# Kernel optimization log

Hardware: AMD Instinct MI355X
Metric: run time of the kernel (lower is better)

## Reference

```python
import jax, jax.numpy as jnp
import numpy as np

V, E, H, D = 10000, 256, 512, 768  # vocab, embed, hidden(=attn), encoder dims
B, T, N = 32, 128, 196


def setup_inputs() -> dict:
    key = jax.random.key(0)
    ks = jax.random.split(key, 16)
    s = 0.02
    inp = {
        "x": jax.random.randint(ks[0], (B, T), 0, V),
        "enc_mem": jax.random.normal(ks[1], (B, N, D), dtype=jnp.float32),
        "enc_mask": jnp.ones((B, N), dtype=jnp.int32),
        # parameters, stored (in, out) so y = x @ W
        "emb_table": jax.random.normal(ks[2], (V, E), dtype=jnp.float32) * s,
        "We": jax.random.normal(ks[3], (D, H), dtype=jnp.float32) * s,   # attn.W_e
        "Wh": jax.random.normal(ks[4], (H, H), dtype=jnp.float32) * s,   # attn.W_h
        "v": jax.random.normal(ks[5], (H,), dtype=jnp.float32) * s,      # attn.v
        "Wih": jax.random.normal(ks[6], (E + D, 4 * H), dtype=jnp.float32) * s,
        "Whh": jax.random.normal(ks[7], (H, 4 * H), dtype=jnp.float32) * s,
        "bih": jnp.zeros((4 * H,), dtype=jnp.float32),
        "bhh": jnp.zeros((4 * H,), dtype=jnp.float32),
        "fcW": jax.random.normal(ks[8], (H, V), dtype=jnp.float32) * s,
        "fcb": jnp.zeros((V,), dtype=jnp.float32),
        "W2h": jax.random.normal(ks[9], (D, H), dtype=jnp.float32) * s,  # enc_to_h
        "b2h": jnp.zeros((H,), dtype=jnp.float32),
        "W2c": jax.random.normal(ks[10], (D, H), dtype=jnp.float32) * s,  # enc_to_c
        "b2c": jnp.zeros((H,), dtype=jnp.float32),
    }
    return inp


def _decode(x, enc_mem, enc_mask, emb_table, We, Wh, v, Wih, Whh, bih, bhh,
            fcW, fcb, W2h, b2h, W2c, b2c):
    emb = emb_table[x]                       # (B,T,E); dropout=0 (eval)
    pooled = enc_mem.mean(axis=1)            # (B,D)
    h = jnp.tanh(pooled @ W2h + b2h)         # init_hidden
    c = jnp.tanh(pooled @ W2c + b2c)
    Ke = jnp.einsum('bnd,dh->bnh', enc_mem, We)  # precompute W_e(enc_mem)
    neg = jnp.float32(-1e9)
    mask0 = (enc_mask == 0)

    def step(carry, e_t):
        h, c = carry
        energy = jnp.tanh((h @ Wh)[:, None, :] + Ke)        # (B,N,H)
        scores = jnp.einsum('bnh,h->bn', energy, v)         # (B,N)
        scores = jnp.where(mask0, neg, scores)
        alpha = jax.nn.softmax(scores, axis=-1)
        context = jnp.einsum('bn,bnd->bd', alpha, enc_mem)  # (B,D)
        lstm_in = jnp.concatenate([e_t, context], axis=-1)  # (B,E+D)
        gates = lstm_in @ Wih + bih + h @ Whh + bhh         # (B,4H)
        i_g, f_g, g_g, o_g = jnp.split(gates, 4, axis=-1)   # torch order i,f,g,o
        c_new = jax.nn.sigmoid(f_g) * c + jax.nn.sigmoid(i_g) * jnp.tanh(g_g)
        h_new = jax.nn.sigmoid(o_g) * jnp.tanh(c_new)
        logit = h_new @ fcW + fcb                           # (B,V)
        return (h_new, c_new), logit

    (h, c), logits_t = jax.lax.scan(step, (h, c), jnp.swapaxes(emb, 0, 1))
    logits = jnp.swapaxes(logits_t, 0, 1)                   # (B,T,V)
    return logits, h, c


def reference(x, enc_mem, enc_mask, emb_table, We, Wh, v, Wih, Whh, bih, bhh,
              fcW, fcb, W2h, b2h, W2c, b2c):
    return _decode(x, enc_mem, enc_mask, emb_table, We, Wh, v, Wih, Whh,
                   bih, bhh, fcW, fcb, W2h, b2h, W2c, b2c)
```

## Files before the change

kernel.cpp:

```cpp
#include <hip/hip_runtime.h>

typedef unsigned short u16;
typedef __attribute__((ext_vector_type(8))) short short8;
typedef __attribute__((ext_vector_type(4))) float f32x4;
typedef __attribute__((ext_vector_type(4))) unsigned int u32x4;

#define B_  32
#define T_  128
#define N_  196
#define D_  768
#define E_  256
#define H_  512
#define V_  10000
#define G4H 2048
#define NBLK 256
#define BH  (B_ * H_)

#define O_ENCBF 0UL
#define O_WHP   9633792UL
#define O_WHHT  10158080UL
#define O_WIHDT 12255232UL
#define O_KE    15400960UL
#define O_GEMB  21823488UL
#define O_BSUM  38600704UL
#define O_CT    38608896UL
#define O_HIST  38674432UL
#define O_HX    42868736UL
#define O_HX2   42999808UL
#define O_HWX   43065344UL
#define O_CTXA  43130880UL
#define O_DEN   43229184UL
#define O_BARS  43229696UL
#define O_REL   43231744UL

__device__ __forceinline__ float b2f(u16 u) {
  union { unsigned i; float f; } c; c.i = ((unsigned)u) << 16; return c.f;
}
__device__ __forceinline__ u16 f2b(float f) {
  unsigned u = __float_as_uint(f);
  unsigned r = (u + 0x7fffu + ((u >> 16) & 1u)) >> 16;
  return (u16)r;
}
__device__ __forceinline__ float fast_tanh(float x) {
  float e = __expf(2.f * x);
  return 1.f - 2.f * __builtin_amdgcn_rcpf(e + 1.f);
}
__device__ __forceinline__ float sigm(float x) {
  return __builtin_amdgcn_rcpf(1.f + __expf(-x));
}
__device__ __forceinline__ float wred_sum(float x) {
  #pragma unroll
  for (int o = 32; o; o >>= 1) x += __shfl_xor(x, o, 64);
  return x;
}

__device__ __forceinline__ float ld_bypass_f32(const float* p) {
  float v;
  asm volatile("global_load_dword %0, %1, off sc0 sc1\n\ts_waitcnt vmcnt(0)"
               : "=v"(v) : "v"(p) : "memory");
  return v;
}
__device__ __forceinline__ unsigned ld_bypass_u32(const unsigned* p) {
  unsigned v;
  asm volatile("global_load_dword %0, %1, off sc0 sc1\n\ts_waitcnt vmcnt(0)"
               : "=v"(v) : "v"(p) : "memory");
  return v;
}
__device__ __forceinline__ void ld2_1_bypass(
    const void* p0, const void* p1, const void* pf,
    u32x4& a, u32x4& b, float& fv) {
  asm volatile(
    "global_load_dwordx4 %0, %3, off sc0 sc1\n\t"
    "global_load_dwordx4 %1, %4, off sc0 sc1\n\t"
    "global_load_dword %2, %5, off sc0 sc1\n\t"
    "s_waitcnt vmcnt(0)"
    : "=&v"(a), "=&v"(b), "=&v"(fv)
    : "v"(p0), "v"(p1), "v"(pf) : "memory");
}
__device__ __forceinline__ void ld6_1_bypass(
    const void* p0, const void* p1, const void* p2, const void* p3,
    const void* p4, const void* p5, const void* pd,
    u32x4& a, u32x4& b, u32x4& c, u32x4& d, u32x4& e, u32x4& f, float& dv) {
  asm volatile(
    "global_load_dwordx4 %0, %7, off sc0 sc1\n\t"
    "global_load_dwordx4 %1, %8, off sc0 sc1\n\t"
    "global_load_dwordx4 %2, %9, off sc0 sc1\n\t"
    "global_load_dwordx4 %3, %10, off sc0 sc1\n\t"
    "global_load_dwordx4 %4, %11, off sc0 sc1\n\t"
    "global_load_dwordx4 %5, %12, off sc0 sc1\n\t"
    "global_load_dword %6, %13, off sc0 sc1\n\t"
    "s_waitcnt vmcnt(0)"
    : "=&v"(a), "=&v"(b), "=&v"(c), "=&v"(d), "=&v"(e), "=&v"(f), "=&v"(dv)
    : "v"(p0), "v"(p1), "v"(p2), "v"(p3), "v"(p4), "v"(p5), "v"(pd)
    : "memory");
}
__device__ __forceinline__ void st_bypass_f32(float* p, float v) {
  asm volatile("global_store_dword %0, %1, off sc0 sc1" :: "v"(p), "v"(v) : "memory");
}
__device__ __forceinline__ void st_bypass_u32(unsigned* p, unsigned v) {
  asm volatile("global_store_dword %0, %1, off sc0 sc1" :: "v"(p), "v"(v) : "memory");
}
__device__ __forceinline__ void st_bypass_u16(u16* p, u16 v) {
  unsigned vv = v;
  asm volatile("global_store_short %0, %1, off sc0 sc1" :: "v"(p), "v"(vv) : "memory");
}

__device__ __forceinline__ unsigned bar_sum16(const unsigned* p) {
  unsigned a0,a1,a2,a3,a4,a5,a6,a7,a8,a9,a10,a11,a12,a13,a14,a15;
  asm volatile(
    "global_load_dword %0, %16, off sc0 sc1\n\t"
    "global_load_dword %1, %16, off offset:128 sc0 sc1\n\t"
    "global_load_dword %2, %16, off offset:256 sc0 sc1\n\t"
    "global_load_dword %3, %16, off offset:384 sc0 sc1\n\t"
    "global_load_dword %4, %16, off offset:512 sc0 sc1\n\t"
    "global_load_dword %5, %16, off offset:640 sc0 sc1\n\t"
    "global_load_dword %6, %16, off offset:768 sc0 sc1\n\t"
    "global_load_dword %7, %16, off offset:896 sc0 sc1\n\t"
    "global_load_dword %8, %16, off offset:1024 sc0 sc1\n\t"
    "global_load_dword %9, %16, off offset:1152 sc0 sc1\n\t"
    "global_load_dword %10, %16, off offset:1280 sc0 sc1\n\t"
    "global_load_dword %11, %16, off offset:1408 sc0 sc1\n\t"
    "global_load_dword %12, %16, off offset:1536 sc0 sc1\n\t"
    "global_load_dword %13, %16, off offset:1664 sc0 sc1\n\t"
    "global_load_dword %14, %16, off offset:1792 sc0 sc1\n\t"
    "global_load_dword %15, %16, off offset:1920 sc0 sc1\n\t"
    "s_waitcnt vmcnt(0)"
    : "=&v"(a0), "=&v"(a1), "=&v"(a2), "=&v"(a3), "=&v"(a4), "=&v"(a5),
      "=&v"(a6), "=&v"(a7), "=&v"(a8), "=&v"(a9), "=&v"(a10), "=&v"(a11),
      "=&v"(a12), "=&v"(a13), "=&v"(a14), "=&v"(a15)
    : "v"(p) : "memory");
  return ((a0+a1)+(a2+a3)) + ((a4+a5)+(a6+a7)) +
         ((a8+a9)+(a10+a11)) + ((a12+a13)+(a14+a15));
}

__device__ __forceinline__ void gridbar(unsigned* bars, unsigned* rel,
                                        int bid, unsigned target) {
  __syncthreads();
  if (bid == 0) {
    if (threadIdx.x == 0) {
      asm volatile("s_waitcnt vmcnt(0) lgkmcnt(0)" ::: "memory");
      __hip_atomic_fetch_add(bars, 1u, __ATOMIC_RELAXED, __HIP_MEMORY_SCOPE_AGENT);
      while (bar_sum16(bars) < target) __builtin_amdgcn_s_sleep(1);
    }
    __syncthreads();
    if (threadIdx.x < NBLK) st_bypass_u32(rel + (size_t)threadIdx.x * 32, target);
  } else {
    if (threadIdx.x == 0) {
      asm volatile("s_waitcnt vmcnt(0) lgkmcnt(0)" ::: "memory");
      __hip_atomic_fetch_add(bars + (size_t)(bid & 15) * 32, 1u,
                             __ATOMIC_RELAXED, __HIP_MEMORY_SCOPE_AGENT);
      while (ld_bypass_u32(rel + (size_t)bid * 32) < target)
        __builtin_amdgcn_s_sleep(2);
    }
    __syncthreads();
  }
}


__global__ void conv_bf(const float* __restrict__ in, u16* __restrict__ out, int n) {
  int i = blockIdx.x * blockDim.x + threadIdx.x;
  int st = gridDim.x * blockDim.x;
  for (; i < n; i += st) out[i] = f2b(in[i]);
}

__global__ void bsum_k(const float* __restrict__ a, const float* __restrict__ b,
                       float* __restrict__ o, int n) {
  int i = blockIdx.x * blockDim.x + threadIdx.x;
  if (i < n) o[i] = a[i] + b[i];
}

__global__ void packw(const float* __restrict__ in, u16* __restrict__ out, int K, int C) {
  int i = blockIdx.x * blockDim.x + threadIdx.x;
  int n = K * C, st = gridDim.x * blockDim.x;
  for (; i < n; i += st) {
    int k = i / C, c = i - k * C;
    out[(((size_t)(k >> 3) * C + c) << 3) + (k & 7)] = f2b(in[i]);
  }
}

__global__ void transpose_bf(const float* __restrict__ in, u16* __restrict__ out, int R, int C) {
  __shared__ float tl[64][65];
  int tid = threadIdx.x;
  int tc0 = blockIdx.x * 64, tr0 = blockIdx.y * 64;
  int cc = tid & 63;
  for (int rr = tid >> 6; rr < 64; rr += 4) {
    int rg = tr0 + rr, cg = tc0 + cc;
    tl[rr][cc] = (rg < R && cg < C) ? in[(size_t)rg * C + cg] : 0.f;
  }
  __syncthreads();
  int rr = tid & 63;
  for (int c2 = tid >> 6; c2 < 64; c2 += 4) {
    int cg = tc0 + c2, rg = tr0 + rr;
    if (cg < C && rg < R) out[(size_t)cg * R + rg] = f2b(tl[rr][c2]);
  }
}

__global__ __launch_bounds__(512) void init_hc(
    const float* __restrict__ enc, const float* __restrict__ W2h,
    const float* __restrict__ b2h, const float* __restrict__ W2c,
    const float* __restrict__ b2c, float* __restrict__ hx,
    u16* __restrict__ hx2, float* __restrict__ cT)
{
  __shared__ float pool[D_];
  int b = blockIdx.x, tid = threadIdx.x;
  for (int d = tid; d < D_; d += 512) {
    float s = 0.f;
    const float* ep = enc + (size_t)b * N_ * D_ + d;
    for (int n = 0; n < N_; ++n) s += ep[(size_t)n * D_];
    pool[d] = s * (1.f / 196.f);
  }
  __syncthreads();
  float a = b2h[tid], a2 = b2c[tid];
  #pragma unroll 4
  for (int d = 0; d < D_; ++d) {
    float pv = pool[d];
    a  += pv * W2h[d * H_ + tid];
    a2 += pv * W2c[d * H_ + tid];
  }
  float h0 = fast_tanh(a);
  hx[b * H_ + tid] = h0;
  hx2[b * H_ + tid] = f2b(h0);
  cT[b * H_ + tid] = fast_tanh(a2);
}

template<int AMODE, int OUTMODE, int BIAS>
__global__ __launch_bounds__(256) void gemm2(
    const void* __restrict__ Av, const float* __restrict__ Bf,
    const int* __restrict__ xidx, void* __restrict__ Cv,
    const float* __restrict__ bias, int M, int N, int K, int lda)
{
  __shared__ __align__(16) u16 Al[128][72];
  __shared__ __align__(16) u16 Bl[128][72];
  const int tid = threadIdx.x;
  const int tm0 = blockIdx.y * 128, tn0 = blockIdx.x * 128;
  const int wv = tid >> 6, lane = tid & 63;
  const int wr = wv >> 1, wc = wv & 1;
  f32x4 acc[4][4] = {};
  const int r = tid >> 1, cb = (tid & 1) * 32;
  const int bkr = tid >> 5;
  const int bnc = (tid & 31) * 4;
  for (int k0 = 0; k0 < K; k0 += 64) {
    int rm = tm0 + r; if (rm >= M) rm = M - 1;
    if (AMODE == 0) {
      const u16* gp = (const u16*)Av + (size_t)rm * lda + k0 + cb;
      #pragma unroll
      for (int u = 0; u < 4; ++u)
        *(short8*)&Al[r][cb + u * 8] = *(const short8*)(gp + u * 8);
    } else {
      const float* gp = (const float*)Av + (size_t)xidx[rm] * lda + k0 + cb;
      #pragma unroll
      for (int u = 0; u < 4; ++u) {
        f32x4 a0 = *(const f32x4*)(gp + u * 8);
        f32x4 a1 = *(const f32x4*)(gp + u * 8 + 4);
        Al[r][cb + u * 8 + 0] = f2b(a0[0]); Al[r][cb + u * 8 + 1] = f2b(a0[1]);
        Al[r][cb + u * 8 + 2] = f2b(a0[2]); Al[r][cb + u * 8 + 3] = f2b(a0[3]);
        Al[r][cb + u * 8 + 4] = f2b(a1[0]); Al[r][cb + u * 8 + 5] = f2b(a1[1]);
        Al[r][cb + u * 8 + 6] = f2b(a1[2]); Al[r][cb + u * 8 + 7] = f2b(a1[3]);
      }
    }
    {
      int ncc = tn0 + bnc; if (ncc > N - 4) ncc = N - 4;
      #pragma unroll
      for (int u = 0; u < 8; ++u) {
        int kr = bkr + u * 8;
        const float* bp = Bf + (size_t)(k0 + kr) * N + ncc;
        f32x4 bv = *(const f32x4*)bp;
        #pragma unroll
        for (int j = 0; j < 4; ++j) Bl[bnc + j][kr] = f2b(bv[j]);
      }
    }
    __syncthreads();
    #pragma unroll
    for (int kk = 0; kk < 64; kk += 32) {
      short8 af[4], bfv[4];
      #pragma unroll
      for (int i = 0; i < 4; ++i)
        af[i] = *(const short8*)&Al[wr * 64 + i * 16 + (lane & 15)][kk + (lane >> 4) * 8];
      #pragma unroll
      for (int j = 0; j < 4; ++j)
        bfv[j] = *(const short8*)&Bl[wc * 64 + j * 16 + (lane & 15)][kk + (lane >> 4) * 8];
      #pragma unroll
      for (int i = 0; i < 4; ++i)
        #pragma unroll
        for (int j = 0; j < 4; ++j)
          acc[i][j] = __builtin_amdgcn_mfma_f32_16x16x32_bf16(af[i], bfv[j], acc[i][j], 0, 0, 0);
    }
    __syncthreads();
  }
  #pragma unroll
  for (int i = 0; i < 4; ++i) {
    int row0 = tm0 + wr * 64 + i * 16 + (lane >> 4) * 4;
    #pragma unroll
    for (int j = 0; j < 4; ++j) {
      int col = tn0 + wc * 64 + j * 16 + (lane & 15);
      if (col < N) {
        float bs = BIAS ? bias[col] : 0.f;
        #pragma unroll
        for (int rr2 = 0; rr2 < 4; ++rr2) {
          int row = row0 + rr2;
          if (row < M) {
            float val = acc[i][j][rr2] + bs;
            if (OUTMODE == 0) ((float*)Cv)[(size_t)row * N + col] = val;
            else if (OUTMODE == 1) ((u16*)Cv)[(size_t)row * N + col] = f2b(val);
            else {
              int tt = row & 127, bb = row >> 7;
              ((u16*)Cv)[((size_t)tt * G4H + col) * 32 + bb] = f2b(val);
            }
          }
        }
      }
    }
  }
}

__global__ __launch_bounds__(512, 1) void recur7(
    const u16* __restrict__ enc_bf, const int* __restrict__ mask,
    const u16* __restrict__ Ke, const u16* __restrict__ Whp,
    const float* __restrict__ vvec, const u16* __restrict__ WhhT,
    const u16* __restrict__ WihDT, const u16* __restrict__ g_emb,
    const float* __restrict__ cT0,
    float* hx, u16* hx2, float* hwx, float* ctxAcc, float* denom,
    u16* h_hist, float* out_h, float* out_c, unsigned* bars, unsigned* rel)
{
  __shared__ u32x4 hst16[64 * 16];
  __shared__ union {
    struct { float h[512]; float part1[8][64]; } p1;
    struct { float hw8[512]; float e[32]; } p2;
    struct { u32x4 ctx16[96 * 16]; f32x4 part3[8][64]; } p3;
  } su;
  __shared__ float gpre[16][16];
  __shared__ float cfl[4][16];
  __shared__ float maskf[32];

  const int bid = blockIdx.x, tid = threadIdx.x;
  const int lane = tid & 63, wvx = tid >> 6;
  const int b = bid >> 3, s8 = bid & 7;
  const int n0 = s8 * 25;
  const int nmax = min(25, N_ - n0);
  const int bh = bid >> 7, hb4 = bid & 127;
  const int b_base = bh * 16, hx4 = hb4 * 4;
  const int n16 = lane & 15, kh = lane >> 4;
  const int gcol = (n16 >> 2) * H_ + hx4 + (n16 & 3);
  const int c_loc = tid & 63, ksW = tid >> 6;
  const int cW = s8 * 64 + c_loc;
  const int bl = tid & 15, kc0 = tid >> 4;
  const int ro = tid & 15, co = tid >> 4;

  float vreg[8];
  #pragma unroll
  for (int j = 0; j < 8; ++j) vreg[j] = vvec[lane * 8 + j];
  if (tid < nmax) maskf[tid] = (mask[b * N_ + n0 + tid] == 0) ? 0.f : 1.f;
  if (tid < 64) cfl[tid >> 4][tid & 15] =
      cT0[(b_base + (tid & 15)) * H_ + hx4 + (tid >> 4)];

  short8 wf[5];
  #pragma unroll
  for (int i = 0; i < 5; ++i) {
    int ks = wvx * 5 + i;
    if (ks < 16) wf[i] = *(const short8*)(WhhT + (size_t)gcol * H_ + ks * 32 + kh * 8);
    else         wf[i] = *(const short8*)(WihDT + (size_t)gcol * D_ + (ks - 16) * 32 + kh * 8);
  }
  short8 whp[8];
  #pragma unroll
  for (int k8 = 0; k8 < 8; ++k8)
    whp[k8] = *(const short8*)(Whp + (((size_t)(ksW * 8 + k8) * H_ + cW) << 3));
  short8 kvp[4];
  #pragma unroll
  for (int i = 0; i < 4; ++i) {
    int nn = wvx + i * 8; if (nn >= nmax) nn = nmax - 1;
    kvp[i] = *(const short8*)(Ke + ((size_t)(b * N_ + n0 + nn)) * H_ + lane * 8);
  }
  __syncthreads();

  unsigned tgt = 0;
  for (int t = 0; t < T_; ++t) {
    const int rb = t & 1, wb = rb ^ 1;
    if (tid < 96) st_bypass_f32(ctxAcc + bid * 96 + tid, 0.f);
    if (bid == 0 && tid < 32) st_bypass_f32(denom + tid, 0.f);
    {
      const u16* hp = hx2 + (size_t)rb * BH + (b_base + bl) * H_;
      u32x4 v0, v1; float hv;
      ld2_1_bypass(hp + kc0 * 8, hp + (kc0 + 32) * 8,
                   hx + (size_t)rb * BH + b * H_ + tid, v0, v1, hv);
      hst16[(kc0     ) * 16 + bl] = v0;
      hst16[(kc0 + 32) * 16 + bl] = v1;
      su.p1.h[tid] = hv;
    }
    __syncthreads();
    {
      float acc = 0.f;
      #pragma unroll
      for (int k8 = 0; k8 < 8; ++k8) {
        short8 w = whp[k8];
        #pragma unroll
        for (int j = 0; j < 8; ++j)
          acc += b2f((u16)w[j]) * su.p1.h[(ksW * 8 + k8) * 8 + j];
      }
      su.p1.part1[ksW][c_loc] = acc;
    }
    __syncthreads();
    if (tid < 64) {
      float s = 0.f;
      #pragma unroll
      for (int w = 0; w < 8; ++w) s += su.p1.part1[w][tid];
      st_bypass_f32(hwx + b * H_ + s8 * 64 + tid, s);
    }
    tgt += NBLK; gridbar(bars, rel, bid, tgt);

    su.p2.hw8[(tid & 7) * 64 + (tid >> 3)] = ld_bypass_f32(hwx + b * H_ + tid);
    __syncthreads();
    #pragma unroll
    for (int i = 0; i < 4; ++i) {
      int nn = wvx + i * 8;
      if (nn < nmax) {
        float p = 0.f;
        #pragma unroll
        for (int j = 0; j < 8; ++j)
          p += vreg[j] * fast_tanh(su.p2.hw8[j * 64 + lane] + b2f((u16)kvp[i][j]));
        p = wred_sum(p);
        if (lane == 0) su.p2.e[nn] = maskf[nn] * __expf(p);
      }
    }
    __syncthreads();
    if (wvx == 0) {
      float sp = (lane < nmax) ? su.p2.e[lane] : 0.f;
      sp = wred_sum(sp);
      if (lane == 0) atomicAdd(denom + b, sp);
    }
    {
      float a0 = 0.f, a1 = 0.f;
      for (int nn = 0; nn < nmax; ++nn) {
        float ev = su.p2.e[nn];
        const u16* ep = enc_bf + ((size_t)(b * N_ + n0 + nn)) * D_;
        a0 += ev * b2f(ep[tid]);
        if (tid < 256) a1 += ev * b2f(ep[512 + tid]);
      }
      atomicAdd(ctxAcc + b * D_ + tid, a0);
      if (tid < 256) atomicAdd(ctxAcc + b * D_ + 512 + tid, a1);
    }
    f32x4 gacc = {0.f, 0.f, 0.f, 0.f};
    #pragma unroll
    for (int i = 0; i < 5; ++i) {
      int ks = wvx * 5 + i;
      if (ks < 16)
        gacc = __builtin_amdgcn_mfma_f32_16x16x32_bf16(
            *(const short8*)&hst16[(ks * 4 + kh) * 16 + n16], wf[i], gacc, 0, 0, 0);
    }
    float ge_pf = 0.f;
    if (tid < 256) {
      int gco = (co >> 2) * H_ + hx4 + (co & 3);
      ge_pf = b2f(g_emb[((size_t)t * G4H + gco) * 32 + (b_base + ro)]);
    }
    tgt += NBLK; gridbar(bars, rel, bid, tgt);

    {
      const float* cp = ctxAcc + (size_t)(b_base + bl) * D_;
      u32x4 ca[3][2]; float dv;
      ld6_1_bypass(cp + (kc0     ) * 8, cp + (kc0     ) * 8 + 4,
                   cp + (kc0 + 32) * 8, cp + (kc0 + 32) * 8 + 4,
                   cp + (kc0 + 64) * 8, cp + (kc0 + 64) * 8 + 4,
                   denom + (b_base + bl),
                   ca[0][0], ca[0][1], ca[1][0], ca[1][1],
                   ca[2][0], ca[2][1], dv);
      float rdv = 1.f / dv;
      #pragma unroll
      for (int r2 = 0; r2 < 3; ++r2) {
        int kc = kc0 + r2 * 32;
        u32x4 pk;
        #pragma unroll
        for (int hh = 0; hh < 2; ++hh) {
          float x0 = __uint_as_float(ca[r2][hh][0]) * rdv;
          float x1 = __uint_as_float(ca[r2][hh][1]) * rdv;
          float x2 = __uint_as_float(ca[r2][hh][2]) * rdv;
          float x3 = __uint_as_float(ca[r2][hh][3]) * rdv;
          pk[hh * 2]     = (unsigned)f2b(x0) | ((unsigned)f2b(x1) << 16);
          pk[hh * 2 + 1] = (unsigned)f2b(x2) | ((unsigned)f2b(x3) << 16);
        }
        su.p3.ctx16[kc * 16 + bl] = pk;
      }
    }
    __syncthreads();
    #pragma unroll
    for (int i = 0; i < 5; ++i) {
      int ks = wvx * 5 + i;
      if (ks >= 16)
        gacc = __builtin_amdgcn_mfma_f32_16x16x32_bf16(
            *(const short8*)&su.p3.ctx16[((ks - 16) * 4 + kh) * 16 + n16], wf[i],
            gacc, 0, 0, 0);
    }
    *(f32x4*)&su.p3.part3[wvx][lane] = gacc;
    __syncthreads();
    if (tid < 256) {
      int lp = ((ro >> 2) << 4) | co;
      float v = su.p3.part3[0][lp][ro & 3] + su.p3.part3[1][lp][ro & 3]
              + su.p3.part3[2][lp][ro & 3] + su.p3.part3[3][lp][ro & 3]
              + su.p3.part3[4][lp][ro & 3] + su.p3.part3[5][lp][ro & 3]
              + su.p3.part3[6][lp][ro & 3] + su.p3.part3[7][lp][ro & 3];
      gpre[co][ro] = v + ge_pf;
    }
    __syncthreads();
    if (tid < 64) {
      int row = tid & 15, j = tid >> 4;
      float gI = gpre[j][row], gF = gpre[4 + j][row];
      float gG = gpre[8 + j][row], gO = gpre[12 + j][row];
      float co2 = cfl[j][row];
      float cn = sigm(gF) * co2 + sigm(gI) * fast_tanh(gG);
      float hn = sigm(gO) * fast_tanh(cn);
      cfl[j][row] = cn;
      int bgl = b_base + row, hidx = hx4 + j;
      st_bypass_f32(hx + (size_t)wb * BH + bgl * H_ + hidx, hn);
      st_bypass_u16(hx2 + (size_t)wb * BH + bgl * H_ + hidx, f2b(hn));
      h_hist[((size_t)(bgl * T_ + t)) * H_ + hidx] = f2b(hn);
      if (t == T_ - 1) {
        out_h[bgl * H_ + hidx] = hn;
        out_c[bgl * H_ + hidx] = cn;
      }
    }
    tgt += NBLK; gridbar(bars, rel, bid, tgt);
  }
}

extern "C" void kernel_launch(void* const* d_in, const int* in_sizes, int n_in,
                              void* d_out, int out_size, void* d_ws, size_t ws_size,
                              hipStream_t stream) {
  const int*   x    = (const int*)d_in[0];
  const float* enc  = (const float*)d_in[1];
  const int*   mask = (const int*)d_in[2];
  const float* emb  = (const float*)d_in[3];
  const float* We   = (const float*)d_in[4];
  const float* Wh   = (const float*)d_in[5];
  const float* v    = (const float*)d_in[6];
  const float* Wih  = (const float*)d_in[7];
  const float* Whh  = (const float*)d_in[8];
  const float* bih  = (const float*)d_in[9];
  const float* bhh  = (const float*)d_in[10];
  const float* fcW  = (const float*)d_in[11];
  const float* fcb  = (const float*)d_in[12];
  const float* W2h  = (const float*)d_in[13];
  const float* b2h  = (const float*)d_in[14];
  const float* W2c  = (const float*)d_in[15];
  const float* b2c  = (const float*)d_in[16];
  float* out = (float*)d_out;

  char* ws = (char*)d_ws;
  u16* enc_bf = (u16*)(ws + O_ENCBF);
  u16* Whp    = (u16*)(ws + O_WHP);
  u16* WhhT   = (u16*)(ws + O_WHHT);
  u16* WihDT  = (u16*)(ws + O_WIHDT);
  u16* Ke     = (u16*)(ws + O_KE);
  u16* g_emb  = (u16*)(ws + O_GEMB);
  float* bsum = (float*)(ws + O_BSUM);
  float* cT   = (float*)(ws + O_CT);
  u16* h_hist = (u16*)(ws + O_HIST);
  float* hx   = (float*)(ws + O_HX);
  u16* hx2    = (u16*)(ws + O_HX2);
  float* hwx  = (float*)(ws + O_HWX);
  float* ctxAcc = (float*)(ws + O_CTXA);
  float* denom  = (float*)(ws + O_DEN);
  unsigned* bars = (unsigned*)(ws + O_BARS);
  unsigned* rel  = (unsigned*)(ws + O_REL);
  float* out_h = out + (size_t)B_ * T_ * V_;
  float* out_c = out_h + B_ * H_;

  hipMemsetAsync(bars, 0, 2048, stream);
  hipMemsetAsync(rel, 0, 32768, stream);
  conv_bf<<<1024, 256, 0, stream>>>(enc, enc_bf, B_ * N_ * D_);
  packw<<<256, 256, 0, stream>>>(Wh, Whp, H_, H_);
  transpose_bf<<<dim3(32, 8), 256, 0, stream>>>(Whh, WhhT, H_, G4H);
  transpose_bf<<<dim3(32, 12), 256, 0, stream>>>(Wih + (size_t)E_ * G4H, WihDT, D_, G4H);
  bsum_k<<<8, 256, 0, stream>>>(bih, bhh, bsum, G4H);
  init_hc<<<32, 512, 0, stream>>>(enc, W2h, b2h, W2c, b2c, hx, hx2, cT);
  gemm2<0, 1, 0><<<dim3(4, 49), 256, 0, stream>>>(enc_bf, We, nullptr, (void*)Ke,
                                                  nullptr, B_ * N_, H_, D_, D_);
  gemm2<1, 3, 1><<<dim3(16, 32), 256, 0, stream>>>(emb, Wih, x, (void*)g_emb,
                                                   bsum, B_ * T_, G4H, E_, E_);
  recur7<<<NBLK, 512, 0, stream>>>(enc_bf, mask, Ke, Whp, v, WhhT, WihDT, g_emb,
                                   cT, hx, hx2, hwx, ctxAcc, denom,
                                   h_hist, out_h, out_c, bars, rel);
  gemm2<0, 0, 1><<<dim3(79, 32), 256, 0, stream>>>(h_hist, fcW, nullptr, (void*)out,
                                                   fcb, B_ * T_, V_, H_, H_);
}
```

Measured before the change: 2.575 ms.

## Compute h@Wh with MFMA on subset of blocks and overlap gate GEMM with grid barriers

The per-step h@Wh projection moves from a scalar FMA reduction in every block, which needed fp32 h and two block syncs, to bf16 MFMA on a quarter of the blocks using a transposed Wh. The recurrent gate MFMA and the g_emb prefetch now run between barrier arrival and the release wait, hiding barrier latency. ctxAcc and denom are double-buffered so the next buffer is zeroed during the end-of-step barrier, which removes the zeroing stores at the start of each step. The context loop packs two bf16 values per load and uses 384 threads. This adds bf16 rounding of h in the attention projection and extra hand-written barrier code.

```diff
diff --git a/kernel.cpp b/kernel.cpp
--- a/kernel.cpp
+++ b/kernel.cpp
@@ -15,9 +15,10 @@
 #define G4H 2048
 #define NBLK 256
 #define BH  (B_ * H_)
+#define BD  (B_ * D_)
 
 #define O_ENCBF 0UL
-#define O_WHP   9633792UL
+#define O_WHT   9633792UL
 #define O_WHHT  10158080UL
 #define O_WIHDT 12255232UL
 #define O_KE    15400960UL
@@ -25,13 +26,12 @@
 #define O_BSUM  38600704UL
 #define O_CT    38608896UL
 #define O_HIST  38674432UL
-#define O_HX    42868736UL
-#define O_HX2   42999808UL
-#define O_HWX   43065344UL
-#define O_CTXA  43130880UL
-#define O_DEN   43229184UL
-#define O_BARS  43229696UL
-#define O_REL   43231744UL
+#define O_HX2   42868736UL
+#define O_HWX   42934272UL
+#define O_CTXA  42999808UL
+#define O_DEN   43196416UL
+#define O_BARS  43196672UL
+#define O_REL   43198720UL
 
 __device__ __forceinline__ float b2f(u16 u) {
   union { unsigned i; float f; } c; c.i = ((unsigned)u) << 16; return c.f;
@@ -66,16 +66,13 @@
                : "=v"(v) : "v"(p) : "memory");
   return v;
 }
-__device__ __forceinline__ void ld2_1_bypass(
-    const void* p0, const void* p1, const void* pf,
-    u32x4& a, u32x4& b, float& fv) {
+__device__ __forceinline__ void ld2_bypass(const void* p0, const void* p1,
+                                           u32x4& a, u32x4& b) {
   asm volatile(
-    "global_load_dwordx4 %0, %3, off sc0 sc1\n\t"
-    "global_load_dwordx4 %1, %4, off sc0 sc1\n\t"
-    "global_load_dword %2, %5, off sc0 sc1\n\t"
+    "global_load_dwordx4 %0, %2, off sc0 sc1\n\t"
+    "global_load_dwordx4 %1, %3, off sc0 sc1\n\t"
     "s_waitcnt vmcnt(0)"
-    : "=&v"(a), "=&v"(b), "=&v"(fv)
-    : "v"(p0), "v"(p1), "v"(pf) : "memory");
+    : "=&v"(a), "=&v"(b) : "v"(p0), "v"(p1) : "memory");
 }
 __device__ __forceinline__ void ld6_1_bypass(
     const void* p0, const void* p1, const void* p2, const void* p3,
@@ -169,15 +166,6 @@
   if (i < n) o[i] = a[i] + b[i];
 }
 
-__global__ void packw(const float* __restrict__ in, u16* __restrict__ out, int K, int C) {
-  int i = blockIdx.x * blockDim.x + threadIdx.x;
-  int n = K * C, st = gridDim.x * blockDim.x;
-  for (; i < n; i += st) {
-    int k = i / C, c = i - k * C;
-    out[(((size_t)(k >> 3) * C + c) << 3) + (k & 7)] = f2b(in[i]);
-  }
-}
-
 __global__ void transpose_bf(const float* __restrict__ in, u16* __restrict__ out, int R, int C) {
   __shared__ float tl[64][65];
   int tid = threadIdx.x;
@@ -198,8 +186,7 @@
 __global__ __launch_bounds__(512) void init_hc(
     const float* __restrict__ enc, const float* __restrict__ W2h,
     const float* __restrict__ b2h, const float* __restrict__ W2c,
-    const float* __restrict__ b2c, float* __restrict__ hx,
-    u16* __restrict__ hx2, float* __restrict__ cT)
+    const float* __restrict__ b2c, u16* __restrict__ hx2, float* __restrict__ cT)
 {
   __shared__ float pool[D_];
   int b = blockIdx.x, tid = threadIdx.x;
@@ -217,9 +204,7 @@
     a  += pv * W2h[d * H_ + tid];
     a2 += pv * W2c[d * H_ + tid];
   }
-  float h0 = fast_tanh(a);
-  hx[b * H_ + tid] = h0;
-  hx2[b * H_ + tid] = f2b(h0);
+  hx2[b * H_ + tid] = f2b(fast_tanh(a));
   cT[b * H_ + tid] = fast_tanh(a2);
 }
 
@@ -313,20 +298,19 @@
   }
 }
 
-__global__ __launch_bounds__(512, 1) void recur7(
+__global__ __launch_bounds__(512, 1) void recur8(
     const u16* __restrict__ enc_bf, const int* __restrict__ mask,
-    const u16* __restrict__ Ke, const u16* __restrict__ Whp,
+    const u16* __restrict__ Ke, const u16* __restrict__ WhT,
     const float* __restrict__ vvec, const u16* __restrict__ WhhT,
     const u16* __restrict__ WihDT, const u16* __restrict__ g_emb,
     const float* __restrict__ cT0,
-    float* hx, u16* hx2, float* hwx, float* ctxAcc, float* denom,
+    u16* hx2, float* hwx, float* ctxAcc, float* denom,
     u16* h_hist, float* out_h, float* out_c, unsigned* bars, unsigned* rel)
 {
   __shared__ u32x4 hst16[64 * 16];
   __shared__ union {
-    struct { float h[512]; float part1[8][64]; } p1;
     struct { float hw8[512]; float e[32]; } p2;
-    struct { u32x4 ctx16[96 * 16]; f32x4 part3[8][64]; } p3;
+    struct { u32x4 ctx16[96 * 16]; f32x4 part3[8][69]; } p3;
   } su;
   __shared__ float gpre[16][16];
   __shared__ float cfl[4][16];
@@ -341,8 +325,8 @@
   const int b_base = bh * 16, hx4 = hb4 * 4;
   const int n16 = lane & 15, kh = lane >> 4;
   const int gcol = (n16 >> 2) * H_ + hx4 + (n16 & 3);
-  const int c_loc = tid & 63, ksW = tid >> 6;
-  const int cW = s8 * 64 + c_loc;
+  const bool is_hw = (bid & 3) == 0;
+  const int c0 = ((bid >> 2) & 31) * 16;
   const int bl = tid & 15, kc0 = tid >> 4;
   const int ro = tid & 15, co = tid >> 4;
 
@@ -360,10 +344,6 @@
     if (ks < 16) wf[i] = *(const short8*)(WhhT + (size_t)gcol * H_ + ks * 32 + kh * 8);
     else         wf[i] = *(const short8*)(WihDT + (size_t)gcol * D_ + (ks - 16) * 32 + kh * 8);
   }
-  short8 whp[8];
-  #pragma unroll
-  for (int k8 = 0; k8 < 8; ++k8)
-    whp[k8] = *(const short8*)(Whp + (((size_t)(ksW * 8 + k8) * H_ + cW) << 3));
   short8 kvp[4];
   #pragma unroll
   for (int i = 0; i < 4; ++i) {
@@ -375,37 +355,70 @@
   unsigned tgt = 0;
   for (int t = 0; t < T_; ++t) {
     const int rb = t & 1, wb = rb ^ 1;
-    if (tid < 96) st_bypass_f32(ctxAcc + bid * 96 + tid, 0.f);
-    if (bid == 0 && tid < 32) st_bypass_f32(denom + tid, 0.f);
+    const int cbuf = t & 1, nbuf = cbuf ^ 1;
     {
       const u16* hp = hx2 + (size_t)rb * BH + (b_base + bl) * H_;
-      u32x4 v0, v1; float hv;
-      ld2_1_bypass(hp + kc0 * 8, hp + (kc0 + 32) * 8,
-                   hx + (size_t)rb * BH + b * H_ + tid, v0, v1, hv);
+      u32x4 v0, v1;
+      ld2_bypass(hp + kc0 * 8, hp + (kc0 + 32) * 8, v0, v1);
       hst16[(kc0     ) * 16 + bl] = v0;
       hst16[(kc0 + 32) * 16 + bl] = v1;
-      su.p1.h[tid] = hv;
-    }
-    __syncthreads();
-    {
-      float acc = 0.f;
-      #pragma unroll
-      for (int k8 = 0; k8 < 8; ++k8) {
-        short8 w = whp[k8];
-        #pragma unroll
-        for (int j = 0; j < 8; ++j)
-          acc += b2f((u16)w[j]) * su.p1.h[(ksW * 8 + k8) * 8 + j];
-      }
-      su.p1.part1[ksW][c_loc] = acc;
-    }
-    __syncthreads();
-    if (tid < 64) {
-      float s = 0.f;
-      #pragma unroll
-      for (int w = 0; w < 8; ++w) s += su.p1.part1[w][tid];
-      st_bypass_f32(hwx + b * H_ + s8 * 64 + tid, s);
-    }
-    tgt += NBLK; gridbar(bars, rel, bid, tgt);
+    }
+    __syncthreads();
+    if (is_hw) {
+      f32x4 hwacc = {0.f, 0.f, 0.f, 0.f};
+      #pragma unroll
+      for (int ks = 0; ks < 16; ++ks) {
+        short8 bfrag = *(const short8*)(WhT + (size_t)(c0 + n16) * H_ + ks * 32 + kh * 8);
+        hwacc = __builtin_amdgcn_mfma_f32_16x16x32_bf16(
+            *(const short8*)&hst16[(ks * 4 + kh) * 16 + n16], bfrag, hwacc, 0, 0, 0);
+      }
+      #pragma unroll
+      for (int j = 0; j < 4; ++j)
+        st_bypass_f32(hwx + (size_t)(b_base + kh * 4 + j) * H_ + c0 + n16, hwacc[j]);
+    }
+    tgt += NBLK;
+    f32x4 gacc = {0.f, 0.f, 0.f, 0.f};
+    float ge_pf = 0.f;
+    __syncthreads();
+    if (tid == 0) {
+      asm volatile("s_waitcnt vmcnt(0) lgkmcnt(0)" ::: "memory");
+      __hip_atomic_fetch_add(bars + (size_t)(bid & 15) * 32, 1u,
+                             __ATOMIC_RELAXED, __HIP_MEMORY_SCOPE_AGENT);
+    }
+    if (bid == 0) {
+      if (tid == 0) { while (bar_sum16(bars) < tgt) __builtin_amdgcn_s_sleep(1); }
+      __syncthreads();
+      if (tid < NBLK) st_bypass_u32(rel + (size_t)tid * 32, tgt);
+      #pragma unroll
+      for (int i = 0; i < 5; ++i) {
+        int ks = wvx * 5 + i;
+        if (ks < 16)
+          gacc = __builtin_amdgcn_mfma_f32_16x16x32_bf16(
+              *(const short8*)&hst16[(ks * 4 + kh) * 16 + n16], wf[i], gacc, 0, 0, 0);
+      }
+      if (tid < 256) {
+        int gco = (co >> 2) * H_ + hx4 + (co & 3);
+        ge_pf = b2f(g_emb[((size_t)t * G4H + gco) * 32 + (b_base + ro)]);
+      }
+    } else {
+      #pragma unroll
+      for (int i = 0; i < 5; ++i) {
+        int ks = wvx * 5 + i;
+        if (ks < 16)
+          gacc = __builtin_amdgcn_mfma_f32_16x16x32_bf16(
+              *(const short8*)&hst16[(ks * 4 + kh) * 16 + n16], wf[i], gacc, 0, 0, 0);
+      }
+      if (tid < 256) {
+        int gco = (co >> 2) * H_ + hx4 + (co & 3);
+        ge_pf = b2f(g_emb[((size_t)t * G4H + gco) * 32 + (b_base + ro)]);
+      }
+      __syncthreads();
+      if (tid == 0) {
+        while (ld_bypass_u32(rel + (size_t)bid * 32) < tgt)
+          __builtin_amdgcn_s_sleep(2);
+      }
+      __syncthreads();
+    }
 
     su.p2.hw8[(tid & 7) * 64 + (tid >> 3)] = ld_bypass_f32(hwx + b * H_ + tid);
     __syncthreads();
@@ -425,41 +438,30 @@
     if (wvx == 0) {
       float sp = (lane < nmax) ? su.p2.e[lane] : 0.f;
       sp = wred_sum(sp);
-      if (lane == 0) atomicAdd(denom + b, sp);
-    }
-    {
+      if (lane == 0) atomicAdd(denom + cbuf * 32 + b, sp);
+    }
+    if (tid < 384) {
       float a0 = 0.f, a1 = 0.f;
+      const u16* ep0 = enc_bf + ((size_t)(b * N_ + n0)) * D_ + 2 * tid;
       for (int nn = 0; nn < nmax; ++nn) {
         float ev = su.p2.e[nn];
-        const u16* ep = enc_bf + ((size_t)(b * N_ + n0 + nn)) * D_;
-        a0 += ev * b2f(ep[tid]);
-        if (tid < 256) a1 += ev * b2f(ep[512 + tid]);
-      }
-      atomicAdd(ctxAcc + b * D_ + tid, a0);
-      if (tid < 256) atomicAdd(ctxAcc + b * D_ + 512 + tid, a1);
-    }
-    f32x4 gacc = {0.f, 0.f, 0.f, 0.f};
-    #pragma unroll
-    for (int i = 0; i < 5; ++i) {
-      int ks = wvx * 5 + i;
-      if (ks < 16)
-        gacc = __builtin_amdgcn_mfma_f32_16x16x32_bf16(
-            *(const short8*)&hst16[(ks * 4 + kh) * 16 + n16], wf[i], gacc, 0, 0, 0);
-    }
-    float ge_pf = 0.f;
-    if (tid < 256) {
-      int gco = (co >> 2) * H_ + hx4 + (co & 3);
-      ge_pf = b2f(g_emb[((size_t)t * G4H + gco) * 32 + (b_base + ro)]);
+        unsigned w = *(const unsigned*)(ep0 + (size_t)nn * D_);
+        a0 += ev * b2f((u16)(w & 0xffffu));
+        a1 += ev * b2f((u16)(w >> 16));
+      }
+      float* cp = ctxAcc + (size_t)cbuf * BD + b * D_ + 2 * tid;
+      atomicAdd(cp, a0);
+      atomicAdd(cp + 1, a1);
     }
     tgt += NBLK; gridbar(bars, rel, bid, tgt);
 
     {
-      const float* cp = ctxAcc + (size_t)(b_base + bl) * D_;
+      const float* cp = ctxAcc + (size_t)cbuf * BD + (size_t)(b_base + bl) * D_;
       u32x4 ca[3][2]; float dv;
       ld6_1_bypass(cp + (kc0     ) * 8, cp + (kc0     ) * 8 + 4,
                    cp + (kc0 + 32) * 8, cp + (kc0 + 32) * 8 + 4,
                    cp + (kc0 + 64) * 8, cp + (kc0 + 64) * 8 + 4,
-                   denom + (b_base + bl),
+                   denom + cbuf * 32 + (b_base + bl),
                    ca[0][0], ca[0][1], ca[1][0], ca[1][1],
                    ca[2][0], ca[2][1], dv);
       float rdv = 1.f / dv;
@@ -508,7 +510,6 @@
       float hn = sigm(gO) * fast_tanh(cn);
       cfl[j][row] = cn;
       int bgl = b_base + row, hidx = hx4 + j;
-      st_bypass_f32(hx + (size_t)wb * BH + bgl * H_ + hidx, hn);
       st_bypass_u16(hx2 + (size_t)wb * BH + bgl * H_ + hidx, f2b(hn));
       h_hist[((size_t)(bgl * T_ + t)) * H_ + hidx] = f2b(hn);
       if (t == T_ - 1) {
@@ -516,7 +517,28 @@
         out_c[bgl * H_ + hidx] = cn;
       }
     }
-    tgt += NBLK; gridbar(bars, rel, bid, tgt);
+    tgt += NBLK;
+    __syncthreads();
+    if (tid == 0) {
+      asm volatile("s_waitcnt vmcnt(0) lgkmcnt(0)" ::: "memory");
+      __hip_atomic_fetch_add(bars + (size_t)(bid & 15) * 32, 1u,
+                             __ATOMIC_RELAXED, __HIP_MEMORY_SCOPE_AGENT);
+    }
+    if (bid == 0) {
+      if (tid == 0) { while (bar_sum16(bars) < tgt) __builtin_amdgcn_s_sleep(1); }
+      __syncthreads();
+      if (tid < NBLK) st_bypass_u32(rel + (size_t)tid * 32, tgt);
+      if (tid < 96) st_bypass_f32(ctxAcc + (size_t)nbuf * BD + bid * 96 + tid, 0.f);
+      if (tid < 32) st_bypass_f32(denom + nbuf * 32 + tid, 0.f);
+    } else {
+      if (tid < 96) st_bypass_f32(ctxAcc + (size_t)nbuf * BD + bid * 96 + tid, 0.f);
+      __syncthreads();
+      if (tid == 0) {
+        while (ld_bypass_u32(rel + (size_t)bid * 32) < tgt)
+          __builtin_amdgcn_s_sleep(2);
+      }
+      __syncthreads();
+    }
   }
 }
 
@@ -544,7 +566,7 @@
 
   char* ws = (char*)d_ws;
   u16* enc_bf = (u16*)(ws + O_ENCBF);
-  u16* Whp    = (u16*)(ws + O_WHP);
+  u16* WhT    = (u16*)(ws + O_WHT);
   u16* WhhT   = (u16*)(ws + O_WHHT);
   u16* WihDT  = (u16*)(ws + O_WIHDT);
   u16* Ke     = (u16*)(ws + O_KE);
@@ -552,7 +574,6 @@
   float* bsum = (float*)(ws + O_BSUM);
   float* cT   = (float*)(ws + O_CT);
   u16* h_hist = (u16*)(ws + O_HIST);
-  float* hx   = (float*)(ws + O_HX);
   u16* hx2    = (u16*)(ws + O_HX2);
   float* hwx  = (float*)(ws + O_HWX);
   float* ctxAcc = (float*)(ws + O_CTXA);
@@ -564,18 +585,20 @@
 
   hipMemsetAsync(bars, 0, 2048, stream);
   hipMemsetAsync(rel, 0, 32768, stream);
+  hipMemsetAsync(ctxAcc, 0, 196608, stream);
+  hipMemsetAsync(denom, 0, 256, stream);
   conv_bf<<<1024, 256, 0, stream>>>(enc, enc_bf, B_ * N_ * D_);
-  packw<<<256, 256, 0, stream>>>(Wh, Whp, H_, H_);
+  transpose_bf<<<dim3(8, 8), 256, 0, stream>>>(Wh, WhT, H_, H_);
   transpose_bf<<<dim3(32, 8), 256, 0, stream>>>(Whh, WhhT, H_, G4H);
   transpose_bf<<<dim3(32, 12), 256, 0, stream>>>(Wih + (size_t)E_ * G4H, WihDT, D_, G4H);
   bsum_k<<<8, 256, 0, stream>>>(bih, bhh, bsum, G4H);
-  init_hc<<<32, 512, 0, stream>>>(enc, W2h, b2h, W2c, b2c, hx, hx2, cT);
+  init_hc<<<32, 512, 0, stream>>>(enc, W2h, b2h, W2c, b2c, hx2, cT);
   gemm2<0, 1, 0><<<dim3(4, 49), 256, 0, stream>>>(enc_bf, We, nullptr, (void*)Ke,
                                                   nullptr, B_ * N_, H_, D_, D_);
   gemm2<1, 3, 1><<<dim3(16, 32), 256, 0, stream>>>(emb, Wih, x, (void*)g_emb,
                                                    bsum, B_ * T_, G4H, E_, E_);
-  recur7<<<NBLK, 512, 0, stream>>>(enc_bf, mask, Ke, Whp, v, WhhT, WihDT, g_emb,
-                                   cT, hx, hx2, hwx, ctxAcc, denom,
+  recur8<<<NBLK, 512, 0, stream>>>(enc_bf, mask, Ke, WhT, v, WhhT, WihDT, g_emb,
+                                   cT, hx2, hwx, ctxAcc, denom,
                                    h_hist, out_h, out_c, bars, rel);
   gemm2<0, 0, 1><<<dim3(79, 32), 256, 0, stream>>>(h_hist, fcW, nullptr, (void*)out,
                                                    fcb, B_ * T_, V_, H_, H_);
```

New measurement: 2.642 ms. 2.6% more time.
